# Performance work log

Measured on AMD Instinct MI355X. Metric: run time of the kernel, lower is better.

Reference implementation:

```python
import jax, jax.numpy as jnp
import numpy as np

B, T, C, H = 8, 2048, 1024, 64

def setup_inputs() -> dict:
    key = jax.random.key(0)
    k0, k1, k2, k3 = jax.random.split(key, 4)
    s = C ** -0.5
    return {
        "x": jax.random.normal(k0, (B, T, C), dtype=jnp.float32),
        "Wq": jax.random.normal(k1, (C, H), dtype=jnp.float32) * s,
        "Wk": jax.random.normal(k2, (C, H), dtype=jnp.float32) * s,
        "Wv": jax.random.normal(k3, (C, H), dtype=jnp.float32) * s,
    }

def reference(x, Wq, Wk, Wv):
    # x: [B,T,C]; Wq/Wk/Wv: [C,H]
    q = jnp.einsum('btc,ch->bth', x, Wq)
    k = jnp.einsum('btc,ch->bth', x, Wk)
    v = jnp.einsum('btc,ch->bth', x, Wv)
    Tn, Cn = x.shape[1], x.shape[2]
    # NOTE: original scales by C**-0.5 (n_embed), not head_size**-0.5
    wei = jnp.einsum('bqh,bkh->bqk', q, k) * (Cn ** -0.5)  # [B,T,T]
    causal = jnp.tril(jnp.ones((Tn, Tn), dtype=bool))
    wei = jnp.where(causal, wei, -jnp.inf)
    wei = jax.nn.softmax(wei, axis=-1)
    # dropout is identity in eval mode
    out = jnp.einsum('bqk,bkh->bqh', wei, v)  # [B,T,H]
    return out
```

## Files before the change

### kernel.cpp

```cpp
#include <hip/hip_runtime.h>
#include <hip/hip_bf16.h>

typedef __attribute__((ext_vector_type(8))) short short8;
typedef __attribute__((ext_vector_type(4))) float f32x4;
typedef __attribute__((ext_vector_type(4))) unsigned short u16x4;
typedef unsigned short u16;

#define Bn 8
#define Tn 2048
#define Cn 1024
#define Hn 64
#define Mrows (Bn * Tn)

#define BARRIER_KEEP_VMCNT() do { \
    asm volatile("s_waitcnt lgkmcnt(0)" ::: "memory"); \
    __builtin_amdgcn_s_barrier(); \
} while (0)

__device__ __forceinline__ u16 bfu(float f) {
    __hip_bfloat16 h = __float2bfloat16(f);
    union { __hip_bfloat16 h; u16 u; } c; c.h = h; return c.u;
}

__device__ __forceinline__ short8 cvt8(f32x4 a0, f32x4 a1) {
    short8 r;
    r[0] = (short)bfu(a0[0]); r[1] = (short)bfu(a0[1]);
    r[2] = (short)bfu(a0[2]); r[3] = (short)bfu(a0[3]);
    r[4] = (short)bfu(a1[0]); r[5] = (short)bfu(a1[1]);
    r[6] = (short)bfu(a1[2]); r[7] = (short)bfu(a1[3]);
    return r;
}

__global__ void convert_w3(const float* __restrict__ Wq, const float* __restrict__ Wk,
                           const float* __restrict__ Wv, u16* __restrict__ wtf, float qscale) {
    int widx = blockIdx.x * 256 + threadIdx.x;
    int mat = widx >> 16;
    int rem = widx & 65535;
    int k = rem >> 6, n = rem & 63;
    const float* W = mat == 0 ? Wq : (mat == 1 ? Wk : Wv);
    float s = mat == 0 ? qscale : 1.0f;
    int ct = mat * 4 + (n >> 4);
    int lane = ((k >> 3) & 3) * 16 + (n & 15);
    wtf[(size_t)(ct * 32 + (k >> 5)) * 512 + lane * 8 + (k & 7)] = bfu(W[rem] * s);
}

__global__ __launch_bounds__(256, 4) void qkv_proj(const float* __restrict__ x,
                                                   const u16* __restrict__ wtf,
                                                   u16* __restrict__ qfl,
                                                   u16* __restrict__ kfl,
                                                   u16* __restrict__ vfl) {
    __shared__ u16 As[2][32][136];
    const int tid = threadIdx.x;
    const int lane = tid & 63;
    const int wn = tid >> 6;
    const int l15 = lane & 15;
    const int lhi = lane >> 4;
    const int row0 = blockIdx.x * 32;

    const int arow = tid >> 3;
    const int ac0 = (tid & 7) * 16;
    const float* asrc = x + (size_t)(row0 + arow) * Cn + ac0;

    f32x4 acc[2][3];
    for (int mt = 0; mt < 2; ++mt)
        for (int nj = 0; nj < 3; ++nj) acc[mt][nj] = f32x4{0.f, 0.f, 0.f, 0.f};

    f32x4 r0 = *(const f32x4*)(asrc);
    f32x4 r1 = *(const f32x4*)(asrc + 4);
    f32x4 r2 = *(const f32x4*)(asrc + 8);
    f32x4 r3 = *(const f32x4*)(asrc + 12);
    *(short8*)&As[0][arow][ac0]     = cvt8(r0, r1);
    *(short8*)&As[0][arow][ac0 + 8] = cvt8(r2, r3);
    r0 = *(const f32x4*)(asrc + 128);
    r1 = *(const f32x4*)(asrc + 132);
    r2 = *(const f32x4*)(asrc + 136);
    r3 = *(const f32x4*)(asrc + 140);
    BARRIER_KEEP_VMCNT();

    for (int ks = 0; ks < 8; ++ks) {
        const int cur = ks & 1;
        if (ks < 7) {
            *(short8*)&As[cur ^ 1][arow][ac0]     = cvt8(r0, r1);
            *(short8*)&As[cur ^ 1][arow][ac0 + 8] = cvt8(r2, r3);
            if (ks < 6) {
                const float* nsrc = asrc + (size_t)(ks + 2) * 128;
                r0 = *(const f32x4*)(nsrc);
                r1 = *(const f32x4*)(nsrc + 4);
                r2 = *(const f32x4*)(nsrc + 8);
                r3 = *(const f32x4*)(nsrc + 12);
            }
        }
        #pragma unroll
        for (int kc = 0; kc < 4; ++kc) {
            short8 af0 = *(const short8*)&As[cur][l15][kc * 32 + lhi * 8];
            short8 af1 = *(const short8*)&As[cur][16 + l15][kc * 32 + lhi * 8];
            #pragma unroll
            for (int nj = 0; nj < 3; ++nj) {
                short8 bf = *(const short8*)(wtf + (size_t)((wn * 3 + nj) * 32 + ks * 4 + kc) * 512 + lane * 8);
                acc[0][nj] = __builtin_amdgcn_mfma_f32_16x16x32_bf16(af0, bf, acc[0][nj], 0, 0, 0);
                acc[1][nj] = __builtin_amdgcn_mfma_f32_16x16x32_bf16(af1, bf, acc[1][nj], 0, 0, 0);
            }
        }
        BARRIER_KEEP_VMCNT();
    }

    for (int mt = 0; mt < 2; ++mt) {
        const int growb = row0 + mt * 16 + lhi * 4;
        const int bI = growb >> 11;
        const int tloc = growb & 2047;
        for (int nj = 0; nj < 3; ++nj) {
            const int gcolb = wn * 48 + nj * 16;
            const int matid = gcolb >> 6;
            const int d0 = gcolb & 63;
            if (matid < 2) {
                u16* dst = matid == 0 ? qfl : kfl;
                const int g = tloc >> 4;
                const int lhid = ((d0 & 31) + l15) >> 3;
                const size_t base = ((size_t)(bI * 128 + g) * 2 + (d0 >> 5)) * 512
                                    + (size_t)lhid * 128 + (l15 & 7);
                for (int r = 0; r < 4; ++r)
                    dst[base + (size_t)(lhi * 4 + r) * 8] = bfu(acc[mt][nj][r]);
            } else {
                const int kt64 = tloc >> 6;
                const int tin = tloc & 63;
                const int kcv = tin >> 5;
                const int lhiv = (tin & 31) >> 3;
                const int e0 = tin & 7;
                const int dt = d0 >> 4;
                u16x4 pk;
                pk[0] = bfu(acc[mt][nj][0]); pk[1] = bfu(acc[mt][nj][1]);
                pk[2] = bfu(acc[mt][nj][2]); pk[3] = bfu(acc[mt][nj][3]);
                *(u16x4*)(vfl + ((size_t)((bI * 32 + kt64) * 4 + dt) * 2 + kcv) * 512
                              + (size_t)(lhiv * 16 + l15) * 8 + e0) = pk;
            }
        }
    }
}

__global__ __launch_bounds__(512, 4) void attn_fwd(const u16* __restrict__ qfl,
                                                   const u16* __restrict__ kfl,
                                                   const u16* __restrict__ vfl,
                                                   float* __restrict__ out) {
    __shared__ float o_lds[8][16][68];
    __shared__ float ml_lds[8][2][16];
    __shared__ u16 pl[8][16][72];
    const int tid = threadIdx.x;
    const int lane = tid & 63;
    const int w = tid >> 6;
    const int l15 = lane & 15, lhi = lane >> 4;
    const int idx = (int)blockIdx.x;
    const int qt = 127 - (idx >> 3);
    const int b = idx & 7;
    const int nkt = (qt >> 2) + 1;
    const int q0 = qt * 16;

    const u16* qb = qfl + (size_t)b * 131072;
    const u16* kb = kfl + (size_t)b * 131072;
    const u16* vb = vfl + (size_t)b * 131072;

    short8 qf[2];
    #pragma unroll
    for (int kc = 0; kc < 2; ++kc)
        qf[kc] = *(const short8*)(qb + ((size_t)(qt * 2 + kc) * 64 + lane) * 8);

    float m = -1e30f, lpart = 0.f;
    f32x4 o[4];
    for (int dt = 0; dt < 4; ++dt) o[dt] = f32x4{0.f, 0.f, 0.f, 0.f};

    for (int kbi = w; kbi < nkt; kbi += 8) {
        const int k0 = kbi * 64;
        short8 kf[2][4], vf[4][2];
        #pragma unroll
        for (int kc = 0; kc < 2; ++kc)
            #pragma unroll
            for (int kt = 0; kt < 4; ++kt)
                kf[kc][kt] = *(const short8*)(kb + ((size_t)((kbi * 4 + kt) * 2 + kc) * 64 + lane) * 8);
        #pragma unroll
        for (int dt = 0; dt < 4; ++dt)
            #pragma unroll
            for (int kc = 0; kc < 2; ++kc)
                vf[dt][kc] = *(const short8*)(vb + ((size_t)((kbi * 4 + dt) * 2 + kc) * 512 + lane * 8));

        f32x4 sacc[4];
        for (int kt = 0; kt < 4; ++kt) sacc[kt] = f32x4{0.f, 0.f, 0.f, 0.f};
        #pragma unroll
        for (int kc = 0; kc < 2; ++kc)
            #pragma unroll
            for (int kt = 0; kt < 4; ++kt)
                sacc[kt] = __builtin_amdgcn_mfma_f32_16x16x32_bf16(kf[kc][kt], qf[kc], sacc[kt], 0, 0, 0);

        if (kbi == nkt - 1) {
            for (int kt = 0; kt < 4; ++kt)
                for (int r = 0; r < 4; ++r) {
                    int kg = k0 + kt * 16 + lhi * 4 + r;
                    if (kg > q0 + l15) sacc[kt][r] = -3.0e38f;
                }
        }
        f32x4 mx0, mx1;
        for (int e = 0; e < 4; ++e) {
            mx0[e] = fmaxf(sacc[0][e], sacc[1][e]);
            mx1[e] = fmaxf(sacc[2][e], sacc[3][e]);
        }
        float tmax = -3.0e38f;
        for (int e = 0; e < 4; ++e) tmax = fmaxf(tmax, fmaxf(mx0[e], mx1[e]));
        tmax = fmaxf(tmax, __shfl_xor(tmax, 16));
        tmax = fmaxf(tmax, __shfl_xor(tmax, 32));
        if (!__all(tmax <= m + 8.0f)) {
            float mnew = fmaxf(m, tmax);
            float corr = exp2f(m - mnew);
            m = mnew;
            lpart *= corr;
            for (int r = 0; r < 4; ++r) {
                float cr = __shfl(corr, lhi * 4 + r);
                for (int dt = 0; dt < 4; ++dt) o[dt][r] *= cr;
            }
        }
        float psum = 0.f;
        for (int kt = 0; kt < 4; ++kt)
            for (int r = 0; r < 4; ++r) {
                float p = exp2f(sacc[kt][r] - m);
                sacc[kt][r] = p;
                psum += p;
            }
        lpart += psum;
        for (int kt = 0; kt < 4; ++kt) {
            u16x4 pk;
            pk[0] = bfu(sacc[kt][0]); pk[1] = bfu(sacc[kt][1]);
            pk[2] = bfu(sacc[kt][2]); pk[3] = bfu(sacc[kt][3]);
            *(u16x4*)&pl[w][l15][kt * 16 + lhi * 4] = pk;
        }
        short8 pf[2];
        #pragma unroll
        for (int kc = 0; kc < 2; ++kc)
            pf[kc] = *(const short8*)&pl[w][l15][kc * 32 + lhi * 8];
        #pragma unroll
        for (int dt = 0; dt < 4; ++dt)
            #pragma unroll
            for (int kc = 0; kc < 2; ++kc)
                o[dt] = __builtin_amdgcn_mfma_f32_16x16x32_bf16(pf[kc], vf[dt][kc], o[dt], 0, 0, 0);
    }
    float lsum = lpart;
    lsum += __shfl_xor(lsum, 16);
    lsum += __shfl_xor(lsum, 32);

    for (int dt = 0; dt < 4; ++dt)
        for (int r = 0; r < 4; ++r)
            o_lds[w][lhi * 4 + r][dt * 16 + l15] = o[dt][r];
    if (lhi == 0) {
        ml_lds[w][0][l15] = m;
        ml_lds[w][1][l15] = lsum;
    }
    __syncthreads();

    float* ob = out + ((size_t)b * Tn + q0) * Hn;
    #pragma unroll
    for (int i = 0; i < 2; ++i) {
        const int e = tid + 512 * i;
        const int row = e >> 6, d = e & 63;
        float M = -3.0e38f;
        #pragma unroll
        for (int ww = 0; ww < 8; ++ww) M = fmaxf(M, ml_lds[ww][0][row]);
        float L = 0.f, acc = 0.f;
        #pragma unroll
        for (int ww = 0; ww < 8; ++ww) {
            float wgt = exp2f(ml_lds[ww][0][row] - M);
            L += ml_lds[ww][1][row] * wgt;
            acc += o_lds[ww][row][d] * wgt;
        }
        ob[(size_t)row * Hn + d] = acc / L;
    }
}

extern "C" void kernel_launch(void* const* d_in, const int* in_sizes, int n_in,
                              void* d_out, int out_size, void* d_ws, size_t ws_size,
                              hipStream_t stream) {
    const float* x = (const float*)d_in[0];
    const float* Wq = (const float*)d_in[1];
    const float* Wk = (const float*)d_in[2];
    const float* Wv = (const float*)d_in[3];
    float* out = (float*)d_out;
    char* ws = (char*)d_ws;

    u16* wtf = (u16*)ws;
    u16* qfl = (u16*)(ws + 196608 * 2);
    u16* kfl = qfl + (size_t)Bn * 131072;
    u16* vfl = kfl + (size_t)Bn * 131072;

    const float qscale = 0.04508422002778011f;
    convert_w3<<<768, 256, 0, stream>>>(Wq, Wk, Wv, wtf, qscale);
    qkv_proj<<<Mrows / 32, 256, 0, stream>>>(x, wtf, qfl, kfl, vfl);
    attn_fwd<<<1024, 512, 0, stream>>>(qfl, kfl, vfl, out);
}
```

Measured before the change: 47.26 us.

## Process two query tiles per block to reuse K/V loads

```diff
diff --git a/kernel.cpp b/kernel.cpp
--- a/kernel.cpp
+++ b/kernel.cpp
@@ -149,125 +149,207 @@
     const int w = tid >> 6;
     const int l15 = lane & 15, lhi = lane >> 4;
     const int idx = (int)blockIdx.x;
-    const int qt = 127 - (idx >> 3);
+    const int j = 63 - (idx >> 3);
     const int b = idx & 7;
-    const int nkt = (qt >> 2) + 1;
-    const int q0 = qt * 16;
+    const int qA = 2 * j, qB = 2 * j + 1;
+    const int nkt = (qB >> 2) + 1;
+    const int q0A = qA * 16, q0B = qB * 16;
 
     const u16* qb = qfl + (size_t)b * 131072;
     const u16* kb = kfl + (size_t)b * 131072;
     const u16* vb = vfl + (size_t)b * 131072;
 
-    short8 qf[2];
+    short8 qfA[2], qfB[2];
     #pragma unroll
-    for (int kc = 0; kc < 2; ++kc)
-        qf[kc] = *(const short8*)(qb + ((size_t)(qt * 2 + kc) * 64 + lane) * 8);
-
-    float m = -1e30f, lpart = 0.f;
-    f32x4 o[4];
-    for (int dt = 0; dt < 4; ++dt) o[dt] = f32x4{0.f, 0.f, 0.f, 0.f};
+    for (int kc = 0; kc < 2; ++kc) {
+        qfA[kc] = *(const short8*)(qb + ((size_t)(qA * 2 + kc) * 64 + lane) * 8);
+        qfB[kc] = *(const short8*)(qb + ((size_t)(qB * 2 + kc) * 64 + lane) * 8);
+    }
+
+    float mA = -1e30f, lA = 0.f, mB = -1e30f, lB = 0.f;
+    f32x4 oA[4], oB[4];
+    for (int dt = 0; dt < 4; ++dt) { oA[dt] = f32x4{0.f, 0.f, 0.f, 0.f}; oB[dt] = oA[dt]; }
 
     for (int kbi = w; kbi < nkt; kbi += 8) {
         const int k0 = kbi * 64;
-        short8 kf[2][4], vf[4][2];
-        #pragma unroll
-        for (int kc = 0; kc < 2; ++kc)
-            #pragma unroll
-            for (int kt = 0; kt < 4; ++kt)
-                kf[kc][kt] = *(const short8*)(kb + ((size_t)((kbi * 4 + kt) * 2 + kc) * 64 + lane) * 8);
+        f32x4 saccA[4], saccB[4];
+        {
+            short8 kf[2][4];
+            #pragma unroll
+            for (int kc = 0; kc < 2; ++kc)
+                #pragma unroll
+                for (int kt = 0; kt < 4; ++kt)
+                    kf[kc][kt] = *(const short8*)(kb + ((size_t)((kbi * 4 + kt) * 2 + kc) * 64 + lane) * 8);
+            for (int kt = 0; kt < 4; ++kt) { saccA[kt] = f32x4{0.f, 0.f, 0.f, 0.f}; saccB[kt] = saccA[kt]; }
+            #pragma unroll
+            for (int kc = 0; kc < 2; ++kc)
+                #pragma unroll
+                for (int kt = 0; kt < 4; ++kt) {
+                    saccA[kt] = __builtin_amdgcn_mfma_f32_16x16x32_bf16(kf[kc][kt], qfA[kc], saccA[kt], 0, 0, 0);
+                    saccB[kt] = __builtin_amdgcn_mfma_f32_16x16x32_bf16(kf[kc][kt], qfB[kc], saccB[kt], 0, 0, 0);
+                }
+        }
+        short8 vf[4][2];
         #pragma unroll
         for (int dt = 0; dt < 4; ++dt)
             #pragma unroll
             for (int kc = 0; kc < 2; ++kc)
                 vf[dt][kc] = *(const short8*)(vb + ((size_t)((kbi * 4 + dt) * 2 + kc) * 512 + lane * 8));
 
-        f32x4 sacc[4];
-        for (int kt = 0; kt < 4; ++kt) sacc[kt] = f32x4{0.f, 0.f, 0.f, 0.f};
-        #pragma unroll
-        for (int kc = 0; kc < 2; ++kc)
-            #pragma unroll
-            for (int kt = 0; kt < 4; ++kt)
-                sacc[kt] = __builtin_amdgcn_mfma_f32_16x16x32_bf16(kf[kc][kt], qf[kc], sacc[kt], 0, 0, 0);
-
-        if (kbi == nkt - 1) {
+        const bool diag = (kbi == nkt - 1);
+        if (diag) {
             for (int kt = 0; kt < 4; ++kt)
                 for (int r = 0; r < 4; ++r) {
                     int kg = k0 + kt * 16 + lhi * 4 + r;
-                    if (kg > q0 + l15) sacc[kt][r] = -3.0e38f;
-                }
-        }
-        f32x4 mx0, mx1;
-        for (int e = 0; e < 4; ++e) {
-            mx0[e] = fmaxf(sacc[0][e], sacc[1][e]);
-            mx1[e] = fmaxf(sacc[2][e], sacc[3][e]);
-        }
-        float tmax = -3.0e38f;
-        for (int e = 0; e < 4; ++e) tmax = fmaxf(tmax, fmaxf(mx0[e], mx1[e]));
-        tmax = fmaxf(tmax, __shfl_xor(tmax, 16));
-        tmax = fmaxf(tmax, __shfl_xor(tmax, 32));
-        if (!__all(tmax <= m + 8.0f)) {
-            float mnew = fmaxf(m, tmax);
-            float corr = exp2f(m - mnew);
-            m = mnew;
-            lpart *= corr;
-            for (int r = 0; r < 4; ++r) {
-                float cr = __shfl(corr, lhi * 4 + r);
-                for (int dt = 0; dt < 4; ++dt) o[dt][r] *= cr;
-            }
-        }
-        float psum = 0.f;
-        for (int kt = 0; kt < 4; ++kt)
-            for (int r = 0; r < 4; ++r) {
-                float p = exp2f(sacc[kt][r] - m);
-                sacc[kt][r] = p;
-                psum += p;
-            }
-        lpart += psum;
-        for (int kt = 0; kt < 4; ++kt) {
-            u16x4 pk;
-            pk[0] = bfu(sacc[kt][0]); pk[1] = bfu(sacc[kt][1]);
-            pk[2] = bfu(sacc[kt][2]); pk[3] = bfu(sacc[kt][3]);
-            *(u16x4*)&pl[w][l15][kt * 16 + lhi * 4] = pk;
-        }
-        short8 pf[2];
-        #pragma unroll
-        for (int kc = 0; kc < 2; ++kc)
-            pf[kc] = *(const short8*)&pl[w][l15][kc * 32 + lhi * 8];
-        #pragma unroll
-        for (int dt = 0; dt < 4; ++dt)
-            #pragma unroll
-            for (int kc = 0; kc < 2; ++kc)
-                o[dt] = __builtin_amdgcn_mfma_f32_16x16x32_bf16(pf[kc], vf[dt][kc], o[dt], 0, 0, 0);
-    }
-    float lsum = lpart;
-    lsum += __shfl_xor(lsum, 16);
-    lsum += __shfl_xor(lsum, 32);
+                    if (kg > q0A + l15) saccA[kt][r] = -3.0e38f;
+                }
+        }
+        {
+            float tmax = -3.0e38f;
+            for (int kt = 0; kt < 4; ++kt)
+                for (int e = 0; e < 4; ++e) tmax = fmaxf(tmax, saccA[kt][e]);
+            tmax = fmaxf(tmax, __shfl_xor(tmax, 16));
+            tmax = fmaxf(tmax, __shfl_xor(tmax, 32));
+            if (!__all(tmax <= mA + 8.0f)) {
+                float mnew = fmaxf(mA, tmax);
+                float corr = exp2f(mA - mnew);
+                mA = mnew; lA *= corr;
+                for (int r = 0; r < 4; ++r) {
+                    float cr = __shfl(corr, lhi * 4 + r);
+                    for (int dt = 0; dt < 4; ++dt) oA[dt][r] *= cr;
+                }
+            }
+            float psum = 0.f;
+            for (int kt = 0; kt < 4; ++kt)
+                for (int r = 0; r < 4; ++r) {
+                    float p = exp2f(saccA[kt][r] - mA);
+                    saccA[kt][r] = p; psum += p;
+                }
+            lA += psum;
+            for (int kt = 0; kt < 4; ++kt) {
+                u16x4 pk;
+                pk[0] = bfu(saccA[kt][0]); pk[1] = bfu(saccA[kt][1]);
+                pk[2] = bfu(saccA[kt][2]); pk[3] = bfu(saccA[kt][3]);
+                *(u16x4*)&pl[w][l15][kt * 16 + lhi * 4] = pk;
+            }
+            short8 pf[2];
+            #pragma unroll
+            for (int kc = 0; kc < 2; ++kc)
+                pf[kc] = *(const short8*)&pl[w][l15][kc * 32 + lhi * 8];
+            #pragma unroll
+            for (int dt = 0; dt < 4; ++dt)
+                #pragma unroll
+                for (int kc = 0; kc < 2; ++kc)
+                    oA[dt] = __builtin_amdgcn_mfma_f32_16x16x32_bf16(pf[kc], vf[dt][kc], oA[dt], 0, 0, 0);
+        }
+        if (diag) {
+            for (int kt = 0; kt < 4; ++kt)
+                for (int r = 0; r < 4; ++r) {
+                    int kg = k0 + kt * 16 + lhi * 4 + r;
+                    if (kg > q0B + l15) saccB[kt][r] = -3.0e38f;
+                }
+        }
+        {
+            float tmax = -3.0e38f;
+            for (int kt = 0; kt < 4; ++kt)
+                for (int e = 0; e < 4; ++e) tmax = fmaxf(tmax, saccB[kt][e]);
+            tmax = fmaxf(tmax, __shfl_xor(tmax, 16));
+            tmax = fmaxf(tmax, __shfl_xor(tmax, 32));
+            if (!__all(tmax <= mB + 8.0f)) {
+                float mnew = fmaxf(mB, tmax);
+                float corr = exp2f(mB - mnew);
+                mB = mnew; lB *= corr;
+                for (int r = 0; r < 4; ++r) {
+                    float cr = __shfl(corr, lhi * 4 + r);
+                    for (int dt = 0; dt < 4; ++dt) oB[dt][r] *= cr;
+                }
+            }
+            float psum = 0.f;
+            for (int kt = 0; kt < 4; ++kt)
+                for (int r = 0; r < 4; ++r) {
+                    float p = exp2f(saccB[kt][r] - mB);
+                    saccB[kt][r] = p; psum += p;
+                }
+            lB += psum;
+            for (int kt = 0; kt < 4; ++kt) {
+                u16x4 pk;
+                pk[0] = bfu(saccB[kt][0]); pk[1] = bfu(saccB[kt][1]);
+                pk[2] = bfu(saccB[kt][2]); pk[3] = bfu(saccB[kt][3]);
+                *(u16x4*)&pl[w][l15][kt * 16 + lhi * 4] = pk;
+            }
+            short8 pf[2];
+            #pragma unroll
+            for (int kc = 0; kc < 2; ++kc)
+                pf[kc] = *(const short8*)&pl[w][l15][kc * 32 + lhi * 8];
+            #pragma unroll
+            for (int dt = 0; dt < 4; ++dt)
+                #pragma unroll
+                for (int kc = 0; kc < 2; ++kc)
+                    oB[dt] = __builtin_amdgcn_mfma_f32_16x16x32_bf16(pf[kc], vf[dt][kc], oB[dt], 0, 0, 0);
+        }
+    }
+
+    float lsA = lA;
+    lsA += __shfl_xor(lsA, 16);
+    lsA += __shfl_xor(lsA, 32);
+    float lsB = lB;
+    lsB += __shfl_xor(lsB, 16);
+    lsB += __shfl_xor(lsB, 32);
 
     for (int dt = 0; dt < 4; ++dt)
         for (int r = 0; r < 4; ++r)
-            o_lds[w][lhi * 4 + r][dt * 16 + l15] = o[dt][r];
+            o_lds[w][lhi * 4 + r][dt * 16 + l15] = oA[dt][r];
     if (lhi == 0) {
-        ml_lds[w][0][l15] = m;
-        ml_lds[w][1][l15] = lsum;
+        ml_lds[w][0][l15] = mA;
+        ml_lds[w][1][l15] = lsA;
     }
     __syncthreads();
-
-    float* ob = out + ((size_t)b * Tn + q0) * Hn;
-    #pragma unroll
-    for (int i = 0; i < 2; ++i) {
-        const int e = tid + 512 * i;
-        const int row = e >> 6, d = e & 63;
-        float M = -3.0e38f;
+    {
+        float* ob = out + ((size_t)b * Tn + q0A) * Hn;
         #pragma unroll
-        for (int ww = 0; ww < 8; ++ww) M = fmaxf(M, ml_lds[ww][0][row]);
-        float L = 0.f, acc = 0.f;
+        for (int i = 0; i < 2; ++i) {
+            const int e = tid + 512 * i;
+            const int row = e >> 6, d = e & 63;
+            float M = -3.0e38f;
+            #pragma unroll
+            for (int ww = 0; ww < 8; ++ww) M = fmaxf(M, ml_lds[ww][0][row]);
+            float L = 0.f, acc = 0.f;
+            #pragma unroll
+            for (int ww = 0; ww < 8; ++ww) {
+                float wgt = exp2f(ml_lds[ww][0][row] - M);
+                L += ml_lds[ww][1][row] * wgt;
+                acc += o_lds[ww][row][d] * wgt;
+            }
+            ob[(size_t)row * Hn + d] = acc / L;
+        }
+    }
+    __syncthreads();
+    for (int dt = 0; dt < 4; ++dt)
+        for (int r = 0; r < 4; ++r)
+            o_lds[w][lhi * 4 + r][dt * 16 + l15] = oB[dt][r];
+    if (lhi == 0) {
+        ml_lds[w][0][l15] = mB;
+        ml_lds[w][1][l15] = lsB;
+    }
+    __syncthreads();
+    {
+        float* ob = out + ((size_t)b * Tn + q0B) * Hn;
         #pragma unroll
-        for (int ww = 0; ww < 8; ++ww) {
-            float wgt = exp2f(ml_lds[ww][0][row] - M);
-            L += ml_lds[ww][1][row] * wgt;
-            acc += o_lds[ww][row][d] * wgt;
-        }
-        ob[(size_t)row * Hn + d] = acc / L;
+        for (int i = 0; i < 2; ++i) {
+            const int e = tid + 512 * i;
+            const int row = e >> 6, d = e & 63;
+            float M = -3.0e38f;
+            #pragma unroll
+            for (int ww = 0; ww < 8; ++ww) M = fmaxf(M, ml_lds[ww][0][row]);
+            float L = 0.f, acc = 0.f;
+            #pragma unroll
+            for (int ww = 0; ww < 8; ++ww) {
+                float wgt = exp2f(ml_lds[ww][0][row] - M);
+                L += ml_lds[ww][1][row] * wgt;
+                acc += o_lds[ww][row][d] * wgt;
+            }
+            ob[(size_t)row * Hn + d] = acc / L;
+        }
     }
 }
 
@@ -289,5 +371,5 @@
     const float qscale = 0.04508422002778011f;
     convert_w3<<<768, 256, 0, stream>>>(Wq, Wk, Wv, wtf, qscale);
     qkv_proj<<<Mrows / 32, 256, 0, stream>>>(x, wtf, qfl, kfl, vfl);
-    attn_fwd<<<1024, 512, 0, stream>>>(qfl, kfl, vfl, out);
-}
+    attn_fwd<<<512, 512, 0, stream>>>(qfl, kfl, vfl, out);
+}
```

After: 75.05 us. 1.59x slower.
